# Performance work log

Measured on AMD Instinct MI355X. Metric: run time of the kernel, lower is better.

Reference implementation:

```python
import jax, jax.numpy as jnp
import numpy as np

N, D, H, C = 100000, 128, 8, 16  # nodes, units=H*C, heads, per-head channels
E = 400000                        # edges per edge set (2 edge sets)
LN_EPS = 1e-3                     # keras LayerNormalization default epsilon


def setup_inputs() -> dict:
    key = jax.random.key(0)
    ks = jax.random.split(key, 16)
    def dense(k, i, o):
        return jax.random.normal(k, (i, o), jnp.float32) / np.float32(np.sqrt(i))
    return dict(
        x=jax.random.normal(ks[0], (N, D), jnp.float32),
        src0=jax.random.randint(ks[1], (E,), 0, N),
        dst0=jax.random.randint(ks[2], (E,), 0, N),
        src1=jax.random.randint(ks[3], (E,), 0, N),
        dst1=jax.random.randint(ks[4], (E,), 0, N),
        Wk=dense(ks[5], D, D), bk=jnp.zeros((D,), jnp.float32),
        Wm=dense(ks[6], D, D), bm=jnp.zeros((D,), jnp.float32),
        Wq=dense(ks[7], D, D), bq=jnp.zeros((D,), jnp.float32),
        Wa=dense(ks[8], D, D), ba=jnp.zeros((D,), jnp.float32),
        Watt0=jax.random.normal(ks[9], (H, C, C), jnp.float32) / np.float32(np.sqrt(C)),
        Wmsg0=jax.random.normal(ks[10], (H, C, C), jnp.float32) / np.float32(np.sqrt(C)),
        Watt1=jax.random.normal(ks[11], (H, C, C), jnp.float32) / np.float32(np.sqrt(C)),
        Wmsg1=jax.random.normal(ks[12], (H, C, C), jnp.float32) / np.float32(np.sqrt(C)),
        prior0=jnp.ones((H,), jnp.float32),
        prior1=jnp.ones((H,), jnp.float32),
        skip=jnp.ones((), jnp.float32),
        gamma=jnp.ones((D,), jnp.float32),
        beta=jnp.zeros((D,), jnp.float32),
    )


def reference(x, src0, dst0, src1, dst1, Wk, bk, Wm, bm, Wq, bq, Wa, ba,
              Watt0, Wmsg0, Watt1, Wmsg1, prior0, prior1, skip, gamma, beta):
    # Node-level projections, split per head: [N, H, C]
    k = (x @ Wk + bk).reshape(N, H, C)
    m = (x @ Wm + bm).reshape(N, H, C)
    q = (x @ Wq + bq).reshape(N, H, C)
    scale = 1.0 / jnp.sqrt(jnp.float32(C))

    def edge_terms(src, dst, Watt, Wmsg, prior):
        # per-edge-type relation projections of gathered sender keys/messages
        ke = jnp.einsum('ehk,hkl->ehl', k[src], Watt)          # [E, H, C]
        score = jnp.einsum('ehl,ehl->eh', ke, q[dst]) * prior * scale  # [E, H]
        msg = jnp.einsum('ehk,hkl->ehl', m[src], Wmsg)          # [E, H, C]
        return score, msg

    s0, m0 = edge_terms(src0, dst0, Watt0, Wmsg0, prior0)
    s1, m1 = edge_terms(src1, dst1, Watt1, Wmsg1, prior1)

    # Joint segment softmax over all incoming edges (both edge sets) per receiver
    scores = jnp.concatenate([s0, s1], axis=0)   # [2E, H]
    msgs = jnp.concatenate([m0, m1], axis=0)     # [2E, H, C]
    recv = jnp.concatenate([dst0, dst1], axis=0)

    smax = jax.ops.segment_max(scores, recv, num_segments=N)   # [N, H]
    ex = jnp.exp(scores - smax[recv])
    denom = jax.ops.segment_sum(ex, recv, num_segments=N)      # [N, H]
    d_e = denom[recv]
    attn = ex / jnp.where(d_e > 0, d_e, 1.0)                   # [2E, H]

    pooled = jax.ops.segment_sum(attn[:, :, None] * msgs, recv,
                                 num_segments=N).reshape(N, D)  # [N, D]

    # aggr(gelu(pooled)); weighted skip; layer norm
    h = jax.nn.gelu(pooled, approximate=False) @ Wa + ba
    alpha = jax.nn.sigmoid(skip)
    out = alpha * h + (1.0 - alpha) * x
    mu = jnp.mean(out, axis=-1, keepdims=True)
    var = jnp.var(out, axis=-1, keepdims=True)
    out = (out - mu) * jax.lax.rsqrt(var + LN_EPS) * gamma + beta
    return out
```

## Files before the change

kernel.cpp:

```cpp
#include <hip/hip_runtime.h>
#include <hip/hip_bf16.h>
#include <math.h>

#define N_NODES 100000
#define DIM 128
#define NH 8
#define NC 16
#define E_EDGES 400000
#define LN_EPS 1e-3f
#define SCAN_B 1024
#define PROJ_GRID 512

typedef __attribute__((ext_vector_type(8))) short short8v;
typedef __attribute__((ext_vector_type(4))) short short4v;
typedef __attribute__((ext_vector_type(4))) float float4v;

__device__ __forceinline__ short bf16bits(float v) {
    __hip_bfloat16 b = __float2bfloat16(v);
    return *(short*)&b;
}

__device__ __forceinline__ void bf2x2(unsigned v, float& a, float& b) {
    a = __uint_as_float(v << 16);
    b = __uint_as_float(v & 0xffff0000u);
}

__global__ __launch_bounds__(128) void fuse_weights(
    const float* __restrict__ Wk, const float* __restrict__ bk,
    const float* __restrict__ Wm, const float* __restrict__ bm,
    const float* __restrict__ Wq, const float* __restrict__ bq,
    const float* __restrict__ Wa, const float* __restrict__ ba,
    const float* __restrict__ Watt0, const float* __restrict__ Wmsg0,
    const float* __restrict__ Watt1, const float* __restrict__ Wmsg1,
    const float* __restrict__ prior0, const float* __restrict__ prior1,
    __hip_bfloat16* __restrict__ Wt, float* __restrict__ bias)
{
    const int c = blockIdx.x;
    const int d = threadIdx.x;
    const int sec = c >> 7, j = c & 127, h = j >> 4, l = j & 15;
    float v, b;
    if (sec == 4)      { v = Wq[d * DIM + j]; b = bq[j]; }
    else if (sec == 5) { v = Wa[d * DIM + j]; b = ba[j]; }
    else {
        const float* W1 = (sec < 2) ? Wk : Wm;
        const float* bs = (sec < 2) ? bk : bm;
        const float* W2 = (sec == 0) ? Watt0 : (sec == 1) ? Watt1
                          : (sec == 2) ? Wmsg0 : Wmsg1;
        float scale = (sec == 0) ? prior0[h] * 0.25f
                    : (sec == 1) ? prior1[h] * 0.25f : 1.f;
        float s = 0.f, sb = 0.f;
        #pragma unroll
        for (int kk = 0; kk < NC; ++kk) {
            float w2 = W2[h * 256 + kk * 16 + l];
            s  = fmaf(W1[d * DIM + h * 16 + kk], w2, s);
            sb = fmaf(bs[h * 16 + kk], w2, sb);
        }
        v = s * scale; b = sb * scale;
    }
    Wt[(size_t)c * DIM + d] = __float2bfloat16(v);
    if (d == 0) bias[c] = b;
}

__global__ __launch_bounds__(512) void proj_mfma(
    const float* __restrict__ x,
    const __hip_bfloat16* __restrict__ Wt,
    const float* __restrict__ bias,
    __hip_bfloat16* __restrict__ km,
    __hip_bfloat16* __restrict__ qb)
{
    __shared__ __align__(16) short xs[2][32 * DIM];
    const int tid = threadIdx.x;
    const int wave = tid >> 6, lane = tid & 63;
    const int quad = lane >> 4, mcol = lane & 15;
    const int nt = N_NODES / 32;

    short8v wf[5][4];
    float4v bv[5];
    #pragma unroll
    for (int s = 0; s < 5; ++s) {
        const int c0 = s * 128 + wave * 16;
        const short* wp = (const short*)Wt + (size_t)(c0 + mcol) * DIM + quad * 8;
        #pragma unroll
        for (int kb = 0; kb < 4; ++kb)
            wf[s][kb] = *(const short8v*)(wp + kb * 32);
        bv[s] = *(const float4v*)(bias + c0 + quad * 4);
    }

    const int srow = tid >> 4, sc8 = tid & 15;
    const int swz = ((sc8 ^ (srow & 7)) * 8);

    int t = blockIdx.x;
    if (t >= nt) return;

    float4v f0 = *(const float4v*)(x + (size_t)(t * 32 + srow) * DIM + sc8 * 8);
    float4v f1 = *(const float4v*)(x + (size_t)(t * 32 + srow) * DIM + sc8 * 8 + 4);
    {
        short8v sv;
        #pragma unroll
        for (int j = 0; j < 4; ++j) { sv[j] = bf16bits(f0[j]); sv[j + 4] = bf16bits(f1[j]); }
        *(short8v*)(xs[0] + srow * DIM + swz) = sv;
    }
    {
        int nn = t + PROJ_GRID;
        if (nn < nt) {
            f0 = *(const float4v*)(x + (size_t)(nn * 32 + srow) * DIM + sc8 * 8);
            f1 = *(const float4v*)(x + (size_t)(nn * 32 + srow) * DIM + sc8 * 8 + 4);
        }
    }

    int cur = 0;
    for (; t < nt; t += PROJ_GRID) {
        __syncthreads();

        short8v b0[4], b1[4];
        #pragma unroll
        for (int kb = 0; kb < 4; ++kb) {
            const int ch = ((quad + kb * 4) ^ (mcol & 7)) * 8;
            b0[kb] = *(const short8v*)(xs[cur] + mcol * DIM + ch);
            b1[kb] = *(const short8v*)(xs[cur] + (mcol + 16) * DIM + ch);
        }

        const int r0 = t * 32;
        #pragma unroll
        for (int s = 0; s < 5; ++s) {
            float4v acc0 = {0.f, 0.f, 0.f, 0.f};
            float4v acc1 = {0.f, 0.f, 0.f, 0.f};
            #pragma unroll
            for (int kb = 0; kb < 4; ++kb) {
                acc0 = __builtin_amdgcn_mfma_f32_16x16x32_bf16(wf[s][kb], b0[kb], acc0, 0, 0, 0);
                acc1 = __builtin_amdgcn_mfma_f32_16x16x32_bf16(wf[s][kb], b1[kb], acc1, 0, 0, 0);
            }
            short4v o0, o1;
            #pragma unroll
            for (int g = 0; g < 4; ++g) {
                o0[g] = bf16bits(acc0[g] + bv[s][g]);
                o1[g] = bf16bits(acc1[g] + bv[s][g]);
            }
            if (s < 4) {
                size_t row = (size_t)(r0 + mcol) + ((s & 1) ? (size_t)N_NODES : 0);
                short* dp = (short*)km + row * 256 + ((s & 2) ? 128 : 0)
                          + wave * 16 + quad * 4;
                *(short4v*)dp              = o0;
                *(short4v*)(dp + 16 * 256) = o1;
            } else {
                short* dp = (short*)qb + (size_t)(r0 + mcol) * DIM
                          + wave * 16 + quad * 4;
                *(short4v*)dp              = o0;
                *(short4v*)(dp + 16 * DIM) = o1;
            }
        }

        int nn = t + PROJ_GRID;
        if (nn < nt) {
            short8v sv;
            #pragma unroll
            for (int j = 0; j < 4; ++j) { sv[j] = bf16bits(f0[j]); sv[j + 4] = bf16bits(f1[j]); }
            *(short8v*)(xs[cur ^ 1] + srow * DIM + swz) = sv;
            int n2 = nn + PROJ_GRID;
            if (n2 < nt) {
                f0 = *(const float4v*)(x + (size_t)(n2 * 32 + srow) * DIM + sc8 * 8);
                f1 = *(const float4v*)(x + (size_t)(n2 * 32 + srow) * DIM + sc8 * 8 + 4);
            }
        }
        cur ^= 1;
    }
}

__global__ __launch_bounds__(256) void hist_kernel(
    const int* __restrict__ dst0, const int* __restrict__ dst1,
    int* __restrict__ counts)
{
    int e = blockIdx.x * 256 + threadIdx.x;
    if (e < E_EDGES) atomicAdd(&counts[dst0[e]], 1);
    int e1 = e - E_EDGES;
    if (e1 >= 0 && e1 < E_EDGES) atomicAdd(&counts[dst1[e1]], 1);
}

__global__ __launch_bounds__(SCAN_B) void scanA_kernel(
    const int* __restrict__ counts, int* __restrict__ row_ptr,
    int* __restrict__ bsum)
{
    __shared__ int buf[2][SCAN_B];
    int i = blockIdx.x * SCAN_B + threadIdx.x;
    int v = (i < N_NODES) ? counts[i] : 0;
    int cur = 0;
    buf[0][threadIdx.x] = v;
    __syncthreads();
    #pragma unroll
    for (int off = 1; off < SCAN_B; off <<= 1) {
        int t = buf[cur][threadIdx.x];
        int add = (threadIdx.x >= off) ? buf[cur][threadIdx.x - off] : 0;
        buf[cur ^ 1][threadIdx.x] = t + add;
        cur ^= 1;
        __syncthreads();
    }
    int inc = buf[cur][threadIdx.x];
    if (i < N_NODES) row_ptr[i] = inc - v;
    if (threadIdx.x == SCAN_B - 1) bsum[blockIdx.x] = inc;
}

__global__ __launch_bounds__(128) void scanB_kernel(int* __restrict__ bsum, int nblocks)
{
    __shared__ int buf[2][128];
    int t = threadIdx.x;
    int v = (t < nblocks) ? bsum[t] : 0;
    buf[0][t] = v;
    __syncthreads();
    int cur = 0;
    #pragma unroll
    for (int off = 1; off < 128; off <<= 1) {
        int a = buf[cur][t];
        if (t >= off) a += buf[cur][t - off];
        buf[cur ^ 1][t] = a;
        cur ^= 1;
        __syncthreads();
    }
    if (t < nblocks) bsum[t] = buf[cur][t] - v;
}

__global__ __launch_bounds__(SCAN_B) void scanC_kernel(
    int* __restrict__ row_ptr, int* __restrict__ cursor,
    const int* __restrict__ bsum)
{
    int i = blockIdx.x * SCAN_B + threadIdx.x;
    if (i < N_NODES) {
        int r = row_ptr[i] + bsum[blockIdx.x];
        row_ptr[i] = r;
        cursor[i] = r;
    }
}

__global__ __launch_bounds__(256) void scatter_kernel(
    const int* __restrict__ src0, const int* __restrict__ dst0,
    const int* __restrict__ src1, const int* __restrict__ dst1,
    int* __restrict__ cursor, unsigned int* __restrict__ eidx)
{
    int e = blockIdx.x * 256 + threadIdx.x;
    if (e < E_EDGES) {
        int d = dst0[e];
        int pos = atomicAdd(&cursor[d], 1);
        eidx[pos] = (unsigned int)src0[e];
    }
    int e1 = e - E_EDGES;
    if (e1 >= 0 && e1 < E_EDGES) {
        int d = dst1[e1];
        int pos = atomicAdd(&cursor[d], 1);
        eidx[pos] = (unsigned int)(src1[e1] + N_NODES);
    }
}

__global__ __launch_bounds__(256) void agg_kernel(
    const uint2* __restrict__ km,
    const uint2* __restrict__ qv,
    const int* __restrict__ row_ptr, const int* __restrict__ counts,
    const unsigned int* __restrict__ eidx,
    unsigned int* __restrict__ pooled)
{
    const int wave = threadIdx.x >> 6, lane = threadIdx.x & 63;
    const int n = blockIdx.x * 4 + wave;
    if (n >= N_NODES) return;
    const int start = row_ptr[n], cnt = counts[n];
    const int low = lane & 31;

    uint2 qu = qv[(size_t)n * 32 + low];
    float q0, q1, q2, q3;
    bf2x2(qu.x, q0, q1); bf2x2(qu.y, q2, q3);

    float a0 = 0.f, a1 = 0.f, a2 = 0.f, a3 = 0.f, den = 0.f;

#define EDGE_ACC(u)                                                          \
    {                                                                        \
        float c0, c1, c2, c3;                                                \
        bf2x2((u).x, c0, c1); bf2x2((u).y, c2, c3);                          \
        float p = fmaf(c3, q3, fmaf(c2, q2, fmaf(c1, q1, c0 * q0)));         \
        p += __shfl_xor(p, 1, 64); p += __shfl_xor(p, 2, 64);                \
        float e = __expf(p);                                                 \
        den += e;                                                            \
        float eb = __shfl_xor(e, 32, 64);                                    \
        a0 = fmaf(eb, c0, a0); a1 = fmaf(eb, c1, a1);                        \
        a2 = fmaf(eb, c2, a2); a3 = fmaf(eb, c3, a3);                        \
    }

    int i = 0;
    for (; i + 4 <= cnt; i += 4) {
        unsigned r0i = eidx[start + i];
        unsigned r1i = eidx[start + i + 1];
        unsigned r2i = eidx[start + i + 2];
        unsigned r3i = eidx[start + i + 3];
        uint2 u0 = km[(size_t)r0i * 64 + lane];
        uint2 u1 = km[(size_t)r1i * 64 + lane];
        uint2 u2 = km[(size_t)r2i * 64 + lane];
        uint2 u3 = km[(size_t)r3i * 64 + lane];
        EDGE_ACC(u0); EDGE_ACC(u1); EDGE_ACC(u2); EDGE_ACC(u3);
    }
    for (; i < cnt; ++i) {
        unsigned r0i = eidx[start + i];
        uint2 u0 = km[(size_t)r0i * 64 + lane];
        EDGE_ACC(u0);
    }
#undef EDGE_ACC

    float denb = __shfl_xor(den, 32, 64);
    float v0 = 0.f, v1 = 0.f, v2 = 0.f, v3 = 0.f;
    if (denb > 0.f) {
        float inv = 1.f / denb;
        v0 = a0 * inv; v1 = a1 * inv; v2 = a2 * inv; v3 = a3 * inv;
    }
    v0 = 0.5f * v0 * (1.f + erff(v0 * 0.70710678118654752f));
    v1 = 0.5f * v1 * (1.f + erff(v1 * 0.70710678118654752f));
    v2 = 0.5f * v2 * (1.f + erff(v2 * 0.70710678118654752f));
    v3 = 0.5f * v3 * (1.f + erff(v3 * 0.70710678118654752f));

    if (lane >= 32) {
        unsigned plo = ((unsigned)(unsigned short)bf16bits(v0))
                     | ((unsigned)(unsigned short)bf16bits(v1) << 16);
        unsigned phi = ((unsigned)(unsigned short)bf16bits(v2))
                     | ((unsigned)(unsigned short)bf16bits(v3) << 16);
        pooled[(size_t)n * 64 + (lane - 32) * 2]     = plo;
        pooled[(size_t)n * 64 + (lane - 32) * 2 + 1] = phi;
    }
}

__global__ __launch_bounds__(256) void final_mfma(
    const __hip_bfloat16* __restrict__ pooled,
    const __hip_bfloat16* __restrict__ Wt,
    const float* __restrict__ bias,
    const float* __restrict__ x,
    const float* __restrict__ skip, const float* __restrict__ gamma,
    const float* __restrict__ beta, float* __restrict__ out)
{
    __shared__ float hs[32][DIM];
    const int wave = threadIdx.x >> 6, lane = threadIdx.x & 63;
    const int quad = lane >> 4, mcol = lane & 15;
    const int r0 = blockIdx.x * 32;

    short8v a0[4], a1[4];
    const short* pp0 = (const short*)pooled + (size_t)(r0 + mcol) * DIM + quad * 8;
    const short* pp1 = pp0 + 16 * DIM;
    #pragma unroll
    for (int kb = 0; kb < 4; ++kb) {
        a0[kb] = *(const short8v*)(pp0 + kb * 32);
        a1[kb] = *(const short8v*)(pp1 + kb * 32);
    }
    const float alpha = 1.f / (1.f + expf(-skip[0]));

    #pragma unroll
    for (int t = 0; t < 2; ++t) {
        const int c0 = wave * 32 + t * 16;
        const short* wp = (const short*)Wt + (size_t)(640 + c0 + mcol) * DIM + quad * 8;
        float4v acc0 = {0.f, 0.f, 0.f, 0.f};
        float4v acc1 = {0.f, 0.f, 0.f, 0.f};
        #pragma unroll
        for (int kb = 0; kb < 4; ++kb) {
            short8v bfr = *(const short8v*)(wp + kb * 32);
            acc0 = __builtin_amdgcn_mfma_f32_16x16x32_bf16(a0[kb], bfr, acc0, 0, 0, 0);
            acc1 = __builtin_amdgcn_mfma_f32_16x16x32_bf16(a1[kb], bfr, acc1, 0, 0, 0);
        }
        const float bcol = bias[640 + c0 + mcol];
        const int cc = c0 + mcol;
        const int rq = quad * 4;
        #pragma unroll
        for (int g = 0; g < 4; ++g) {
            int rA = rq + g, rB = rq + 16 + g;
            hs[rA][cc] = alpha * (acc0[g] + bcol)
                       + (1.f - alpha) * x[(size_t)(r0 + rA) * DIM + cc];
            hs[rB][cc] = alpha * (acc1[g] + bcol)
                       + (1.f - alpha) * x[(size_t)(r0 + rB) * DIM + cc];
        }
    }
    __syncthreads();

    float gam0 = gamma[lane], gam1 = gamma[lane + 64];
    float bet0 = beta[lane],  bet1 = beta[lane + 64];
    for (int r = wave; r < 32; r += 4) {
        int row = r0 + r;
        float v0 = hs[r][lane], v1 = hs[r][lane + 64];
        float s = v0 + v1, s2 = v0 * v0 + v1 * v1;
        #pragma unroll
        for (int off = 1; off < 64; off <<= 1) {
            s  += __shfl_xor(s,  off, 64);
            s2 += __shfl_xor(s2, off, 64);
        }
        float mu = s * (1.f / 128.f);
        float var = s2 * (1.f / 128.f) - mu * mu;
        float rstd = rsqrtf(var + LN_EPS);
        out[(size_t)row * DIM + lane]      = (v0 - mu) * rstd * gam0 + bet0;
        out[(size_t)row * DIM + lane + 64] = (v1 - mu) * rstd * gam1 + bet1;
    }
}

extern "C" void kernel_launch(void* const* d_in, const int* in_sizes, int n_in,
                              void* d_out, int out_size, void* d_ws, size_t ws_size,
                              hipStream_t stream) {
    const float* x     = (const float*)d_in[0];
    const int*   src0  = (const int*)d_in[1];
    const int*   dst0  = (const int*)d_in[2];
    const int*   src1  = (const int*)d_in[3];
    const int*   dst1  = (const int*)d_in[4];
    const float* Wk    = (const float*)d_in[5];
    const float* bk    = (const float*)d_in[6];
    const float* Wm    = (const float*)d_in[7];
    const float* bm    = (const float*)d_in[8];
    const float* Wq    = (const float*)d_in[9];
    const float* bq    = (const float*)d_in[10];
    const float* Wa    = (const float*)d_in[11];
    const float* ba    = (const float*)d_in[12];
    const float* Watt0 = (const float*)d_in[13];
    const float* Wmsg0 = (const float*)d_in[14];
    const float* Watt1 = (const float*)d_in[15];
    const float* Wmsg1 = (const float*)d_in[16];
    const float* prior0= (const float*)d_in[17];
    const float* prior1= (const float*)d_in[18];
    const float* skip  = (const float*)d_in[19];
    const float* gamma = (const float*)d_in[20];
    const float* beta  = (const float*)d_in[21];
    float* out = (float*)d_out;

    const size_t nd = (size_t)N_NODES * DIM;
    char* wsb = (char*)d_ws;
    __hip_bfloat16* Wt    = (__hip_bfloat16*)wsb;  wsb += (size_t)768 * DIM * 2;
    float* bias           = (float*)wsb;           wsb += 768 * 4;
    __hip_bfloat16* km    = (__hip_bfloat16*)wsb;  wsb += (size_t)2 * N_NODES * 256 * 2;
    __hip_bfloat16* qb    = (__hip_bfloat16*)wsb;  wsb += nd * 2;
    __hip_bfloat16* pooled= (__hip_bfloat16*)wsb;  wsb += nd * 2;
    int* counts  = (int*)wsb;                      wsb += (size_t)N_NODES * 4;
    int* row_ptr = (int*)wsb;                      wsb += (size_t)N_NODES * 4;
    int* cursor  = (int*)wsb;                      wsb += (size_t)N_NODES * 4;
    int* bsum    = (int*)wsb;                      wsb += 128 * 4;
    unsigned int* eidx = (unsigned int*)wsb;

    hipMemsetAsync(counts, 0, (size_t)N_NODES * 4, stream);

    const int scan_blocks = (N_NODES + SCAN_B - 1) / SCAN_B;
    const int edge_blocks = (2 * E_EDGES + 255) / 256;

    hist_kernel<<<dim3(edge_blocks), dim3(256), 0, stream>>>(dst0, dst1, counts);
    scanA_kernel<<<dim3(scan_blocks), dim3(SCAN_B), 0, stream>>>(counts, row_ptr, bsum);
    scanB_kernel<<<dim3(1), dim3(128), 0, stream>>>(bsum, scan_blocks);
    scanC_kernel<<<dim3(scan_blocks), dim3(SCAN_B), 0, stream>>>(row_ptr, cursor, bsum);
    scatter_kernel<<<dim3(edge_blocks), dim3(256), 0, stream>>>(
        src0, dst0, src1, dst1, cursor, eidx);

    fuse_weights<<<dim3(768), dim3(128), 0, stream>>>(
        Wk, bk, Wm, bm, Wq, bq, Wa, ba,
        Watt0, Wmsg0, Watt1, Wmsg1, prior0, prior1, Wt, bias);
    proj_mfma<<<dim3(PROJ_GRID), dim3(512), 0, stream>>>(
        x, Wt, bias, km, qb);

    agg_kernel<<<dim3((N_NODES + 3) / 4), dim3(256), 0, stream>>>(
        (const uint2*)km, (const uint2*)qb, row_ptr, counts, eidx,
        (unsigned int*)pooled);

    final_mfma<<<dim3(N_NODES / 32), dim3(256), 0, stream>>>(
        pooled, Wt, bias, x, skip, gamma, beta, out);
}
```

Measured before the change: 370.5 us.

## Interleave key and message per lane in km rows so each lane computes full edges

```diff
diff --git a/kernel.cpp b/kernel.cpp
--- a/kernel.cpp
+++ b/kernel.cpp
@@ -121,33 +121,50 @@
         }
 
         const int r0 = t * 32;
-        #pragma unroll
-        for (int s = 0; s < 5; ++s) {
-            float4v acc0 = {0.f, 0.f, 0.f, 0.f};
-            float4v acc1 = {0.f, 0.f, 0.f, 0.f};
+        const int colb = wave * 32 + quad * 8;
+
+        #pragma unroll
+        for (int e = 0; e < 2; ++e) {
+            float4v aK0 = {0.f,0.f,0.f,0.f}, aK1 = {0.f,0.f,0.f,0.f};
+            float4v aM0 = {0.f,0.f,0.f,0.f}, aM1 = {0.f,0.f,0.f,0.f};
             #pragma unroll
             for (int kb = 0; kb < 4; ++kb) {
-                acc0 = __builtin_amdgcn_mfma_f32_16x16x32_bf16(wf[s][kb], b0[kb], acc0, 0, 0, 0);
-                acc1 = __builtin_amdgcn_mfma_f32_16x16x32_bf16(wf[s][kb], b1[kb], acc1, 0, 0, 0);
+                aK0 = __builtin_amdgcn_mfma_f32_16x16x32_bf16(wf[e][kb],     b0[kb], aK0, 0, 0, 0);
+                aK1 = __builtin_amdgcn_mfma_f32_16x16x32_bf16(wf[e][kb],     b1[kb], aK1, 0, 0, 0);
+                aM0 = __builtin_amdgcn_mfma_f32_16x16x32_bf16(wf[2 + e][kb], b0[kb], aM0, 0, 0, 0);
+                aM1 = __builtin_amdgcn_mfma_f32_16x16x32_bf16(wf[2 + e][kb], b1[kb], aM1, 0, 0, 0);
+            }
+            short8v o0, o1;
+            #pragma unroll
+            for (int g = 0; g < 4; ++g) {
+                const int pos = (g & 2) * 2 + (g & 1);
+                o0[pos]     = bf16bits(aK0[g] + bv[e][g]);
+                o0[pos + 2] = bf16bits(aM0[g] + bv[2 + e][g]);
+                o1[pos]     = bf16bits(aK1[g] + bv[e][g]);
+                o1[pos + 2] = bf16bits(aM1[g] + bv[2 + e][g]);
+            }
+            short* dp = (short*)km
+                      + ((size_t)(r0 + mcol) + (size_t)e * N_NODES) * 256 + colb;
+            *(short8v*)dp              = o0;
+            *(short8v*)(dp + 16 * 256) = o1;
+        }
+
+        {
+            float4v a0v = {0.f,0.f,0.f,0.f}, a1v = {0.f,0.f,0.f,0.f};
+            #pragma unroll
+            for (int kb = 0; kb < 4; ++kb) {
+                a0v = __builtin_amdgcn_mfma_f32_16x16x32_bf16(wf[4][kb], b0[kb], a0v, 0, 0, 0);
+                a1v = __builtin_amdgcn_mfma_f32_16x16x32_bf16(wf[4][kb], b1[kb], a1v, 0, 0, 0);
             }
             short4v o0, o1;
             #pragma unroll
             for (int g = 0; g < 4; ++g) {
-                o0[g] = bf16bits(acc0[g] + bv[s][g]);
-                o1[g] = bf16bits(acc1[g] + bv[s][g]);
+                o0[g] = bf16bits(a0v[g] + bv[4][g]);
+                o1[g] = bf16bits(a1v[g] + bv[4][g]);
             }
-            if (s < 4) {
-                size_t row = (size_t)(r0 + mcol) + ((s & 1) ? (size_t)N_NODES : 0);
-                short* dp = (short*)km + row * 256 + ((s & 2) ? 128 : 0)
-                          + wave * 16 + quad * 4;
-                *(short4v*)dp              = o0;
-                *(short4v*)(dp + 16 * 256) = o1;
-            } else {
-                short* dp = (short*)qb + (size_t)(r0 + mcol) * DIM
-                          + wave * 16 + quad * 4;
-                *(short4v*)dp              = o0;
-                *(short4v*)(dp + 16 * DIM) = o1;
-            }
+            short* dp = (short*)qb + (size_t)(r0 + mcol) * DIM + wave * 16 + quad * 4;
+            *(short4v*)dp              = o0;
+            *(short4v*)(dp + 16 * DIM) = o1;
         }
 
         int nn = t + PROJ_GRID;
@@ -250,8 +267,8 @@
 }
 
 __global__ __launch_bounds__(256) void agg_kernel(
-    const uint2* __restrict__ km,
-    const uint2* __restrict__ qv,
+    const char* __restrict__ km,
+    const unsigned* __restrict__ qv,
     const int* __restrict__ row_ptr, const int* __restrict__ counts,
     const unsigned int* __restrict__ eidx,
     unsigned int* __restrict__ pooled)
@@ -260,25 +277,24 @@
     const int n = blockIdx.x * 4 + wave;
     if (n >= N_NODES) return;
     const int start = row_ptr[n], cnt = counts[n];
-    const int low = lane & 31;
-
-    uint2 qu = qv[(size_t)n * 32 + low];
-    float q0, q1, q2, q3;
-    bf2x2(qu.x, q0, q1); bf2x2(qu.y, q2, q3);
-
-    float a0 = 0.f, a1 = 0.f, a2 = 0.f, a3 = 0.f, den = 0.f;
+    const unsigned lane8 = (unsigned)lane << 3;
+
+    unsigned qu = qv[(size_t)n * 64 + lane];
+    float q0, q1; bf2x2(qu, q0, q1);
+
+    float a0 = 0.f, a1 = 0.f, den = 0.f;
 
 #define EDGE_ACC(u)                                                          \
     {                                                                        \
-        float c0, c1, c2, c3;                                                \
-        bf2x2((u).x, c0, c1); bf2x2((u).y, c2, c3);                          \
-        float p = fmaf(c3, q3, fmaf(c2, q2, fmaf(c1, q1, c0 * q0)));         \
-        p += __shfl_xor(p, 1, 64); p += __shfl_xor(p, 2, 64);                \
+        float k0, k1, m0, m1;                                                \
+        bf2x2((u).x, k0, k1); bf2x2((u).y, m0, m1);                          \
+        float p = fmaf(k1, q1, k0 * q0);                                     \
+        p += __shfl_xor(p, 1, 64);                                           \
+        p += __shfl_xor(p, 2, 64);                                           \
+        p += __shfl_xor(p, 4, 64);                                           \
         float e = __expf(p);                                                 \
         den += e;                                                            \
-        float eb = __shfl_xor(e, 32, 64);                                    \
-        a0 = fmaf(eb, c0, a0); a1 = fmaf(eb, c1, a1);                        \
-        a2 = fmaf(eb, c2, a2); a3 = fmaf(eb, c3, a3);                        \
+        a0 = fmaf(e, m0, a0); a1 = fmaf(e, m1, a1);                          \
     }
 
     int i = 0;
@@ -287,38 +303,30 @@
         unsigned r1i = eidx[start + i + 1];
         unsigned r2i = eidx[start + i + 2];
         unsigned r3i = eidx[start + i + 3];
-        uint2 u0 = km[(size_t)r0i * 64 + lane];
-        uint2 u1 = km[(size_t)r1i * 64 + lane];
-        uint2 u2 = km[(size_t)r2i * 64 + lane];
-        uint2 u3 = km[(size_t)r3i * 64 + lane];
+        uint2 u0 = *(const uint2*)(km + ((r0i << 9) | lane8));
+        uint2 u1 = *(const uint2*)(km + ((r1i << 9) | lane8));
+        uint2 u2 = *(const uint2*)(km + ((r2i << 9) | lane8));
+        uint2 u3 = *(const uint2*)(km + ((r3i << 9) | lane8));
         EDGE_ACC(u0); EDGE_ACC(u1); EDGE_ACC(u2); EDGE_ACC(u3);
     }
     for (; i < cnt; ++i) {
         unsigned r0i = eidx[start + i];
-        uint2 u0 = km[(size_t)r0i * 64 + lane];
+        uint2 u0 = *(const uint2*)(km + ((r0i << 9) | lane8));
         EDGE_ACC(u0);
     }
 #undef EDGE_ACC
 
-    float denb = __shfl_xor(den, 32, 64);
-    float v0 = 0.f, v1 = 0.f, v2 = 0.f, v3 = 0.f;
-    if (denb > 0.f) {
-        float inv = 1.f / denb;
-        v0 = a0 * inv; v1 = a1 * inv; v2 = a2 * inv; v3 = a3 * inv;
+    float v0 = 0.f, v1 = 0.f;
+    if (den > 0.f) {
+        float inv = 1.f / den;
+        v0 = a0 * inv; v1 = a1 * inv;
     }
     v0 = 0.5f * v0 * (1.f + erff(v0 * 0.70710678118654752f));
     v1 = 0.5f * v1 * (1.f + erff(v1 * 0.70710678118654752f));
-    v2 = 0.5f * v2 * (1.f + erff(v2 * 0.70710678118654752f));
-    v3 = 0.5f * v3 * (1.f + erff(v3 * 0.70710678118654752f));
-
-    if (lane >= 32) {
-        unsigned plo = ((unsigned)(unsigned short)bf16bits(v0))
-                     | ((unsigned)(unsigned short)bf16bits(v1) << 16);
-        unsigned phi = ((unsigned)(unsigned short)bf16bits(v2))
-                     | ((unsigned)(unsigned short)bf16bits(v3) << 16);
-        pooled[(size_t)n * 64 + (lane - 32) * 2]     = plo;
-        pooled[(size_t)n * 64 + (lane - 32) * 2 + 1] = phi;
-    }
+
+    unsigned packed = ((unsigned)(unsigned short)bf16bits(v0))
+                    | ((unsigned)(unsigned short)bf16bits(v1) << 16);
+    pooled[(size_t)n * 64 + lane] = packed;
 }
 
 __global__ __launch_bounds__(256) void final_mfma(
@@ -448,7 +456,7 @@
         x, Wt, bias, km, qb);
 
     agg_kernel<<<dim3((N_NODES + 3) / 4), dim3(256), 0, stream>>>(
-        (const uint2*)km, (const uint2*)qb, row_ptr, counts, eidx,
+        (const char*)km, (const unsigned*)qb, row_ptr, counts, eidx,
         (unsigned int*)pooled);
 
     final_mfma<<<dim3(N_NODES / 32), dim3(256), 0, stream>>>(
```

After: 357.4 us. -3.5%, faster.
